# Optimization experiments

Measured on AMD Instinct MI355X. Metric: run time of the kernel, lower is better.

The kernel has to match this reference:

```python
import jax, jax.numpy as jnp
from jax import lax
import numpy as np

T, B, I, H = 512, 1024, 64, 64


def setup_inputs() -> dict:
    key = jax.random.key(0)
    k1, k2, k3, k4, k5 = jax.random.split(key, 5)
    s = 1.0 / np.sqrt(H)  # PyTorch GRU init scale
    X = jax.random.normal(k1, (T, B, I), dtype=jnp.float32)
    W_ih = jax.random.uniform(k2, (3 * H, I), jnp.float32, -s, s)
    W_hh = jax.random.uniform(k3, (3 * H, H), jnp.float32, -s, s)
    b_ih = jax.random.uniform(k4, (3 * H,), jnp.float32, -s, s)
    b_hh = jax.random.uniform(k5, (3 * H,), jnp.float32, -s, s)
    return {"X": X, "W_ih": W_ih, "W_hh": W_hh, "b_ih": b_ih, "b_hh": b_hh}


def reference(X, W_ih, W_hh, b_ih, b_hh):
    # Single-layer GRU, PyTorch semantics, gate order (r, z, n), h0 = 0.
    Hh = W_hh.shape[1]
    # Precompute input-side gate projections for all timesteps: [T, B, 3H]
    gates_x = jnp.einsum('tbi,gi->tbg', X, W_ih) + b_ih

    def step(h, gx):
        gh = h @ W_hh.T + b_hh  # [B, 3H]
        r = jax.nn.sigmoid(gx[:, :Hh] + gh[:, :Hh])
        z = jax.nn.sigmoid(gx[:, Hh:2 * Hh] + gh[:, Hh:2 * Hh])
        n = jnp.tanh(gx[:, 2 * Hh:] + r * gh[:, 2 * Hh:])
        h_new = (1.0 - z) * n + z * h
        return h_new, h_new

    h0 = jnp.zeros((X.shape[1], Hh), dtype=X.dtype)
    h_last, output = lax.scan(step, h0, gates_x)
    return output, h_last[None]  # ([T,B,H], [1,B,H])
```

## Files before the change

### kernel.cpp

```cpp
#include <hip/hip_runtime.h>


typedef _Float16 half8  __attribute__((ext_vector_type(8)));
typedef __fp16   fp16x2 __attribute__((ext_vector_type(2)));
typedef float    f32x4  __attribute__((ext_vector_type(4)));
typedef int      i32x4  __attribute__((ext_vector_type(4)));

#define T_STEPS 512
#define BATCH   1024
#define LOG2E   1.4426950408889634f

struct XBuf { float4 a0, a1, b0, b1; };

__device__ __forceinline__ int pk2(float x, float y) {
    fp16x2 p = __builtin_amdgcn_cvt_pkrtz(x, y);
    return __builtin_bit_cast(int, p);
}

__device__ __forceinline__ half8 cvt8p(const float4& a, const float4& b) {
    i32x4 v;
    v[0] = pk2(a.x, a.y); v[1] = pk2(a.z, a.w);
    v[2] = pk2(b.x, b.y); v[3] = pk2(b.z, b.w);
    return __builtin_bit_cast(half8, v);
}

__device__ __forceinline__ half8 loadw8s(const float* p, float s) {
    const float4* q = (const float4*)p;
    float4 a = q[0], b = q[1];
    half8 h;
    h[0] = (_Float16)(a.x * s); h[1] = (_Float16)(a.y * s);
    h[2] = (_Float16)(a.z * s); h[3] = (_Float16)(a.w * s);
    h[4] = (_Float16)(b.x * s); h[5] = (_Float16)(b.y * s);
    h[6] = (_Float16)(b.z * s); h[7] = (_Float16)(b.w * s);
    return h;
}

__device__ __forceinline__ void block_sync() {
    asm volatile("s_waitcnt lgkmcnt(0)" ::: "memory");
    __builtin_amdgcn_s_barrier();
    asm volatile("" ::: "memory");
}

#define MFMA16(A, B, C) __builtin_amdgcn_mfma_f32_16x16x32_f16((A), (B), (C), 0, 0, 0)

__global__ __launch_bounds__(256, 1)
void gru_fused_kernel(const float* __restrict__ X,
                      const float* __restrict__ W_ih,
                      const float* __restrict__ W_hh,
                      const float* __restrict__ b_ih,
                      const float* __restrict__ b_hh,
                      float* __restrict__ out)
{
    const int tid   = threadIdx.x;
    const int wq    = tid >> 6;
    const int l     = tid & 63;
    const int c     = l & 15;
    const int g4    = l >> 4;
    const int u     = wq * 16 + c;
    const int brow0 = blockIdx.x * 16;

    __shared__ __align__(16) _Float16 hbuf[2][16][72];

    const float sRZ = -LOG2E;
    const float sN  = 2.0f * LOG2E;

    const half8 Brx0 = loadw8s(W_ih + (u)       * 64 +      8 * g4, sRZ);
    const half8 Brx1 = loadw8s(W_ih + (u)       * 64 + 32 + 8 * g4, sRZ);
    const half8 Bzx0 = loadw8s(W_ih + (64 + u)  * 64 +      8 * g4, sRZ);
    const half8 Bzx1 = loadw8s(W_ih + (64 + u)  * 64 + 32 + 8 * g4, sRZ);
    const half8 Bnx0 = loadw8s(W_ih + (128 + u) * 64 +      8 * g4, sN);
    const half8 Bnx1 = loadw8s(W_ih + (128 + u) * 64 + 32 + 8 * g4, sN);
    const half8 Brh0 = loadw8s(W_hh + (u)       * 64 +      8 * g4, sRZ);
    const half8 Brh1 = loadw8s(W_hh + (u)       * 64 + 32 + 8 * g4, sRZ);
    const half8 Bzh0 = loadw8s(W_hh + (64 + u)  * 64 +      8 * g4, sRZ);
    const half8 Bzh1 = loadw8s(W_hh + (64 + u)  * 64 + 32 + 8 * g4, sRZ);
    const half8 Bnh0 = loadw8s(W_hh + (128 + u) * 64 +      8 * g4, sN);
    const half8 Bnh1 = loadw8s(W_hh + (128 + u) * 64 + 32 + 8 * g4, sN);

    const float rb  = sRZ * (b_ih[u]      + b_hh[u]);
    const float zb  = sRZ * (b_ih[64 + u] + b_hh[64 + u]);
    const float nxb = sN * b_ih[128 + u];
    const float nhb = sN * b_hh[128 + u];

    const f32x4 rb4  = {rb, rb, rb, rb};
    const f32x4 zb4  = {zb, zb, zb, zb};
    const f32x4 nxb4 = {nxb, nxb, nxb, nxb};
    const f32x4 nhb4 = {nhb, nhb, nhb, nhb};
    const f32x4 z4   = {0.f, 0.f, 0.f, 0.f};

    const int xlane = (brow0 + c) * 64 + 8 * g4;
    float* outp = out + (size_t)((brow0 + 4 * g4) * 64 + u);

#define ISSUE_X(XB, TN) do {                                                  \
        const float* px_ = X + (size_t)(TN) * (BATCH * 64) + xlane;           \
        const float4* q_ = (const float4*)px_;                                \
        (XB).a0 = q_[0]; (XB).a1 = q_[1];                                     \
        (XB).b0 = q_[8]; (XB).b1 = q_[9];                                     \
    } while (0)

    XBuf xb0, xb1;
    ISSUE_X(xb0, 0);
    ISSUE_X(xb1, 1);

    for (int k = tid; k < 2 * 16 * 72; k += 256)
        ((_Float16*)hbuf)[k] = (_Float16)0.f;
    __syncthreads();

    f32x4 hp = {0.f, 0.f, 0.f, 0.f};

#define STEP(T, P, XA) do {                                                   \
                    \
        const half8 hf0 = *(const half8*)&hbuf[P][c][8 * g4];                 \
        const half8 hf1 = *(const half8*)&hbuf[P][c][32 + 8 * g4];            \
        const half8 xf0 = cvt8p((XA).a0, (XA).a1);                            \
        const half8 xf1 = cvt8p((XA).b0, (XA).b1);                            \
        { int tn_ = (T) + 2; if (tn_ > T_STEPS - 1) tn_ = T_STEPS - 1;        \
          ISSUE_X(XA, tn_); }                                                 \
            \
        f32x4 crx = MFMA16(xf0, Brx0, rb4);  crx = MFMA16(xf1, Brx1, crx);    \
        f32x4 czx = MFMA16(xf0, Bzx0, zb4);  czx = MFMA16(xf1, Bzx1, czx);    \
        f32x4 cnx = MFMA16(xf0, Bnx0, nxb4); cnx = MFMA16(xf1, Bnx1, cnx);    \
          \
        const f32x4 crh0 = MFMA16(hf0, Brh0, z4);                             \
        const f32x4 crh1 = MFMA16(hf1, Brh1, z4);                             \
        const f32x4 czh0 = MFMA16(hf0, Bzh0, z4);                             \
        const f32x4 czh1 = MFMA16(hf1, Bzh1, z4);                             \
        const f32x4 cnh0 = MFMA16(hf0, Bnh0, nhb4);                           \
        const f32x4 cnh1 = MFMA16(hf1, Bnh1, z4);                             \
        _Pragma("unroll")                                                     \
        for (int i = 0; i < 4; ++i) {                                         \
            const float cr  = (crx[i] + crh0[i]) + crh1[i];                   \
            const float cz  = (czx[i] + czh0[i]) + czh1[i];                   \
            const float cnh = cnh0[i] + cnh1[i];                              \
            const float rv = __builtin_amdgcn_rcpf(                           \
                                 1.f + __builtin_amdgcn_exp2f(cr));           \
            const float zv = __builtin_amdgcn_rcpf(                           \
                                 1.f + __builtin_amdgcn_exp2f(cz));           \
            const float npre = fmaf(rv, cnh, cnx[i]);                         \
            const float e  = __builtin_amdgcn_exp2f(npre);                    \
            const float nv = 1.f - 2.f * __builtin_amdgcn_rcpf(e + 1.f);      \
            const float hn = fmaf(zv, hp[i] - nv, nv);                        \
            hp[i] = hn;                                                       \
            hbuf[(P) ^ 1][4 * g4 + i][u] = (_Float16)hn;                      \
            outp[i * 64] = hn;                                                \
        }                                                                     \
        outp += BATCH * 64;                                                   \
        block_sync();                                                         \
    } while (0)

    #pragma unroll 1
    for (int t = 0; t < T_STEPS; t += 2) {
        STEP(t,     0, xb0);
        STEP(t + 1, 1, xb1);
    }

    #pragma unroll
    for (int i = 0; i < 4; ++i)
        outp[i * 64] = hp[i];

#undef STEP
#undef ISSUE_X
}

extern "C" void kernel_launch(void* const* d_in, const int* in_sizes, int n_in,
                              void* d_out, int out_size, void* d_ws, size_t ws_size,
                              hipStream_t stream) {
    const float* X    = (const float*)d_in[0];
    const float* W_ih = (const float*)d_in[1];
    const float* W_hh = (const float*)d_in[2];
    const float* b_ih = (const float*)d_in[3];
    const float* b_hh = (const float*)d_in[4];
    float* out = (float*)d_out;

    gru_fused_kernel<<<dim3(BATCH / 16), dim3(256), 0, stream>>>(
        X, W_ih, W_hh, b_ih, b_hh, out);
}
```

Baseline: 324.9 us.

## Swap MFMA operands so each lane holds four hidden units of one batch row

The weights now feed the MFMA A operand and x/h feed the B operand, which transposes the output tile. Each lane ends up with four consecutive hidden units for one batch row. The recurrent MFMAs accumulate directly into the input-side accumulators, removing separate zero-init partials and the scalar adds. Per-lane results are written as one packed 8-byte LDS store and one 16-byte global store instead of four scattered scalar stores. Biases become per-element vectors loaded with float4; the serial MFMA accumulation chain is longer, which could add latency on the recurrent critical path.

After: 383.3 us. +18.0%, slower.

```diff
diff --git a/kernel.cpp b/kernel.cpp
--- a/kernel.cpp
+++ b/kernel.cpp
@@ -56,7 +56,8 @@
     const int l     = tid & 63;
     const int c     = l & 15;
     const int g4    = l >> 4;
-    const int u     = wq * 16 + c;
+    const int ar    = 16 * wq + c;
+    const int ub    = 16 * wq + 4 * g4;
     const int brow0 = blockIdx.x * 16;
 
     __shared__ __align__(16) _Float16 hbuf[2][16][72];
@@ -64,32 +65,37 @@
     const float sRZ = -LOG2E;
     const float sN  = 2.0f * LOG2E;
 
-    const half8 Brx0 = loadw8s(W_ih + (u)       * 64 +      8 * g4, sRZ);
-    const half8 Brx1 = loadw8s(W_ih + (u)       * 64 + 32 + 8 * g4, sRZ);
-    const half8 Bzx0 = loadw8s(W_ih + (64 + u)  * 64 +      8 * g4, sRZ);
-    const half8 Bzx1 = loadw8s(W_ih + (64 + u)  * 64 + 32 + 8 * g4, sRZ);
-    const half8 Bnx0 = loadw8s(W_ih + (128 + u) * 64 +      8 * g4, sN);
-    const half8 Bnx1 = loadw8s(W_ih + (128 + u) * 64 + 32 + 8 * g4, sN);
-    const half8 Brh0 = loadw8s(W_hh + (u)       * 64 +      8 * g4, sRZ);
-    const half8 Brh1 = loadw8s(W_hh + (u)       * 64 + 32 + 8 * g4, sRZ);
-    const half8 Bzh0 = loadw8s(W_hh + (64 + u)  * 64 +      8 * g4, sRZ);
-    const half8 Bzh1 = loadw8s(W_hh + (64 + u)  * 64 + 32 + 8 * g4, sRZ);
-    const half8 Bnh0 = loadw8s(W_hh + (128 + u) * 64 +      8 * g4, sN);
-    const half8 Bnh1 = loadw8s(W_hh + (128 + u) * 64 + 32 + 8 * g4, sN);
+    const half8 Arx0 = loadw8s(W_ih + (ar)       * 64 +      8 * g4, sRZ);
+    const half8 Arx1 = loadw8s(W_ih + (ar)       * 64 + 32 + 8 * g4, sRZ);
+    const half8 Azx0 = loadw8s(W_ih + (64 + ar)  * 64 +      8 * g4, sRZ);
+    const half8 Azx1 = loadw8s(W_ih + (64 + ar)  * 64 + 32 + 8 * g4, sRZ);
+    const half8 Anx0 = loadw8s(W_ih + (128 + ar) * 64 +      8 * g4, sN);
+    const half8 Anx1 = loadw8s(W_ih + (128 + ar) * 64 + 32 + 8 * g4, sN);
+    const half8 Arh0 = loadw8s(W_hh + (ar)       * 64 +      8 * g4, sRZ);
+    const half8 Arh1 = loadw8s(W_hh + (ar)       * 64 + 32 + 8 * g4, sRZ);
+    const half8 Azh0 = loadw8s(W_hh + (64 + ar)  * 64 +      8 * g4, sRZ);
+    const half8 Azh1 = loadw8s(W_hh + (64 + ar)  * 64 + 32 + 8 * g4, sRZ);
+    const half8 Anh0 = loadw8s(W_hh + (128 + ar) * 64 +      8 * g4, sN);
+    const half8 Anh1 = loadw8s(W_hh + (128 + ar) * 64 + 32 + 8 * g4, sN);
 
-    const float rb  = sRZ * (b_ih[u]      + b_hh[u]);
-    const float zb  = sRZ * (b_ih[64 + u] + b_hh[64 + u]);
-    const float nxb = sN * b_ih[128 + u];
-    const float nhb = sN * b_hh[128 + u];
-
-    const f32x4 rb4  = {rb, rb, rb, rb};
-    const f32x4 zb4  = {zb, zb, zb, zb};
-    const f32x4 nxb4 = {nxb, nxb, nxb, nxb};
-    const f32x4 nhb4 = {nhb, nhb, nhb, nhb};
-    const f32x4 z4   = {0.f, 0.f, 0.f, 0.f};
+    const float4 bir = *(const float4*)(b_ih + ub);
+    const float4 bhr = *(const float4*)(b_hh + ub);
+    const float4 biz = *(const float4*)(b_ih + 64 + ub);
+    const float4 bhz = *(const float4*)(b_hh + 64 + ub);
+    const float4 bin = *(const float4*)(b_ih + 128 + ub);
+    const float4 bhn = *(const float4*)(b_hh + 128 + ub);
+    f32x4 rb4, zb4, nxb4, nhb4;
+    rb4[0] = sRZ * (bir.x + bhr.x); rb4[1] = sRZ * (bir.y + bhr.y);
+    rb4[2] = sRZ * (bir.z + bhr.z); rb4[3] = sRZ * (bir.w + bhr.w);
+    zb4[0] = sRZ * (biz.x + bhz.x); zb4[1] = sRZ * (biz.y + bhz.y);
+    zb4[2] = sRZ * (biz.z + bhz.z); zb4[3] = sRZ * (biz.w + bhz.w);
+    nxb4[0] = sN * bin.x; nxb4[1] = sN * bin.y;
+    nxb4[2] = sN * bin.z; nxb4[3] = sN * bin.w;
+    nhb4[0] = sN * bhn.x; nhb4[1] = sN * bhn.y;
+    nhb4[2] = sN * bhn.z; nhb4[3] = sN * bhn.w;
 
     const int xlane = (brow0 + c) * 64 + 8 * g4;
-    float* outp = out + (size_t)((brow0 + 4 * g4) * 64 + u);
+    float* outp = out + (size_t)((brow0 + c) * 64 + ub);
 
 #define ISSUE_X(XB, TN) do {                                                  \
         const float* px_ = X + (size_t)(TN) * (BATCH * 64) + xlane;           \
@@ -109,41 +115,47 @@
     f32x4 hp = {0.f, 0.f, 0.f, 0.f};
 
 #define STEP(T, P, XA) do {                                                   \
-                    \
+                   \
         const half8 hf0 = *(const half8*)&hbuf[P][c][8 * g4];                 \
         const half8 hf1 = *(const half8*)&hbuf[P][c][32 + 8 * g4];            \
         const half8 xf0 = cvt8p((XA).a0, (XA).a1);                            \
         const half8 xf1 = cvt8p((XA).b0, (XA).b1);                            \
         { int tn_ = (T) + 2; if (tn_ > T_STEPS - 1) tn_ = T_STEPS - 1;        \
           ISSUE_X(XA, tn_); }                                                 \
-            \
-        f32x4 crx = MFMA16(xf0, Brx0, rb4);  crx = MFMA16(xf1, Brx1, crx);    \
-        f32x4 czx = MFMA16(xf0, Bzx0, zb4);  czx = MFMA16(xf1, Bzx1, czx);    \
-        f32x4 cnx = MFMA16(xf0, Bnx0, nxb4); cnx = MFMA16(xf1, Bnx1, cnx);    \
-          \
-        const f32x4 crh0 = MFMA16(hf0, Brh0, z4);                             \
-        const f32x4 crh1 = MFMA16(hf1, Brh1, z4);                             \
-        const f32x4 czh0 = MFMA16(hf0, Bzh0, z4);                             \
-        const f32x4 czh1 = MFMA16(hf1, Bzh1, z4);                             \
-        const f32x4 cnh0 = MFMA16(hf0, Bnh0, nhb4);                           \
-        const f32x4 cnh1 = MFMA16(hf1, Bnh1, z4);                             \
+                \
+        f32x4 cr  = MFMA16(Arx0, xf0, rb4);                                   \
+        cr        = MFMA16(Arx1, xf1, cr);                                    \
+        f32x4 cz  = MFMA16(Azx0, xf0, zb4);                                   \
+        cz        = MFMA16(Azx1, xf1, cz);                                    \
+        f32x4 cnx = MFMA16(Anx0, xf0, nxb4);                                  \
+        cnx       = MFMA16(Anx1, xf1, cnx);                                   \
+        cr        = MFMA16(Arh0, hf0, cr);                                    \
+        cr        = MFMA16(Arh1, hf1, cr);                                    \
+        cz        = MFMA16(Azh0, hf0, cz);                                    \
+        cz        = MFMA16(Azh1, hf1, cz);                                    \
+        f32x4 cnh = MFMA16(Anh0, hf0, nhb4);                                  \
+        cnh       = MFMA16(Anh1, hf1, cnh);                                   \
+        f32x4 hn4;                                                            \
         _Pragma("unroll")                                                     \
         for (int i = 0; i < 4; ++i) {                                         \
-            const float cr  = (crx[i] + crh0[i]) + crh1[i];                   \
-            const float cz  = (czx[i] + czh0[i]) + czh1[i];                   \
-            const float cnh = cnh0[i] + cnh1[i];                              \
             const float rv = __builtin_amdgcn_rcpf(                           \
-                                 1.f + __builtin_amdgcn_exp2f(cr));           \
+                                 1.f + __builtin_amdgcn_exp2f(cr[i]));        \
             const float zv = __builtin_amdgcn_rcpf(                           \
-                                 1.f + __builtin_amdgcn_exp2f(cz));           \
-            const float npre = fmaf(rv, cnh, cnx[i]);                         \
+                                 1.f + __builtin_amdgcn_exp2f(cz[i]));        \
+            const float npre = fmaf(rv, cnh[i], cnx[i]);                      \
             const float e  = __builtin_amdgcn_exp2f(npre);                    \
             const float nv = 1.f - 2.f * __builtin_amdgcn_rcpf(e + 1.f);      \
             const float hn = fmaf(zv, hp[i] - nv, nv);                        \
             hp[i] = hn;                                                       \
-            hbuf[(P) ^ 1][4 * g4 + i][u] = (_Float16)hn;                      \
-            outp[i * 64] = hn;                                                \
+            hn4[i] = hn;                                                      \
         }                                                                     \
+                           \
+        { uint2 hw;                                                           \
+          hw.x = (unsigned)pk2(hn4[0], hn4[1]);                               \
+          hw.y = (unsigned)pk2(hn4[2], hn4[3]);                               \
+          *(uint2*)&hbuf[(P) ^ 1][c][ub] = hw; }                              \
+                                                \
+        *(f32x4*)outp = hn4;                                                  \
         outp += BATCH * 64;                                                   \
         block_sync();                                                         \
     } while (0)
@@ -154,9 +166,7 @@
         STEP(t + 1, 1, xb1);
     }
 
-    #pragma unroll
-    for (int i = 0; i < 4; ++i)
-        outp[i * 64] = hp[i];
+    *(f32x4*)outp = hp;
 
 #undef STEP
 #undef ISSUE_X
```
